# Optimization experiments

Hardware: AMD Instinct MI355X
Metric: run time of the kernel (lower is better)

Reference implementation:

```python
import jax, jax.numpy as jnp
from jax import lax
import numpy as np

B = 2
N_PER = 12000
TIMES = 16
C_IN = 4
# sparse_shape = grid_size[::-1] + [1,0,0], grid_size=[160,160,40]
S1 = (41, 160, 160)
S2 = (21, 80, 80)   # conv2: k3 s2 p1
S3 = (11, 40, 40)   # conv3: k3 s2 p1
S4 = (5, 20, 20)    # conv4: k3 s2 p(0,1,1)
SOUT = (2, 20, 20)  # conv_out: k(3,1,1) s(2,1,1) p0
# per-BN-layer channel counts, flattened into gamma/beta vectors
CH = [16, 16, 32, 32, 32, 64, 64, 64, 64, 64, 64, 128]
OFF = np.concatenate([[0], np.cumsum(CH)]).tolist()


def _downsample_coords(coords, in_shape, k, s, p):
    # spconv SparseConv3d output index rule: output j active iff some active
    # input x satisfies j*s - p <= x <= j*s - p + k - 1 within bounds.
    out_shape = np.array([(in_shape[i] + 2 * p[i] - k[i]) // s[i] + 1 for i in range(3)])
    b, xs = coords[:, :1], coords[:, 1:]
    s_arr = np.array(s)
    cand = []
    for o0 in range(k[0]):
        for o1 in range(k[1]):
            for o2 in range(k[2]):
                j = xs + np.array([p[0] - o0, p[1] - o1, p[2] - o2])
                ok = np.all(j % s_arr == 0, axis=1)
                jj = j // s_arr
                ok &= np.all((jj >= 0) & (jj < out_shape), axis=1)
                cand.append(np.concatenate([b[ok], jj[ok]], axis=1))
    return np.unique(np.concatenate(cand, axis=0), axis=0).astype(np.int32)


def _make_coords():
    rng = np.random.default_rng(0)
    ncell = S1[0] * S1[1] * S1[2]
    per = []
    for b in range(B):
        flat = rng.choice(ncell, size=N_PER, replace=False)
        z, y, x = np.unravel_index(flat, S1)
        per.append(np.stack([np.full(N_PER, b), z, y, x], axis=1))
    c1 = np.concatenate(per, axis=0).astype(np.int32)
    c2 = _downsample_coords(c1, S1, (3, 3, 3), (2, 2, 2), (1, 1, 1))
    c3 = _downsample_coords(c2, S2, (3, 3, 3), (2, 2, 2), (1, 1, 1))
    c4 = _downsample_coords(c3, S3, (3, 3, 3), (2, 2, 2), (0, 1, 1))
    c5 = _downsample_coords(c4, S4, (3, 1, 1), (2, 1, 1), (0, 0, 0))
    return c1, c2, c3, c4, c5


def _w(key, shape):
    fan_in = shape[0] * shape[1] * shape[2] * shape[3]
    return jax.random.normal(key, shape, jnp.float32) * np.float32(np.sqrt(2.0 / fan_in))


def setup_inputs():
    c1, c2, c3, c4, c5 = _make_coords()
    ks = jax.random.split(jax.random.key(0), 16)
    t = TIMES
    return {
        "voxel_features": jax.random.normal(ks[0], (c1.shape[0], C_IN), jnp.float32),
        "w_in": _w(ks[1], (3, 3, 3, C_IN, t)),
        "w1": _w(ks[2], (3, 3, 3, t, t)),
        "w2_0": _w(ks[3], (3, 3, 3, t, 2 * t)),
        "w2_1": _w(ks[4], (3, 3, 3, 2 * t, 2 * t)),
        "w2_2": _w(ks[5], (3, 3, 3, 2 * t, 2 * t)),
        "w3_0": _w(ks[6], (3, 3, 3, 2 * t, 4 * t)),
        "w3_1": _w(ks[7], (3, 3, 3, 4 * t, 4 * t)),
        "w3_2": _w(ks[8], (3, 3, 3, 4 * t, 4 * t)),
        "w4_0": _w(ks[9], (3, 3, 3, 4 * t, 4 * t)),
        "w4_1": _w(ks[10], (3, 3, 3, 4 * t, 4 * t)),
        "w4_2": _w(ks[11], (3, 3, 3, 4 * t, 4 * t)),
        "w_out": _w(ks[12], (3, 1, 1, 4 * t, 8 * t)),
        "gamma": 1.0 + 0.1 * jax.random.normal(ks[13], (sum(CH),), jnp.float32),
        "beta": 0.1 * jax.random.normal(ks[14], (sum(CH),), jnp.float32),
        "coords1": jnp.asarray(c1), "coords2": jnp.asarray(c2),
        "coords3": jnp.asarray(c3), "coords4": jnp.asarray(c4),
        "coords_out": jnp.asarray(c5),
    }


def _sp_conv(feats, in_coords, w, in_shape, out_coords, stride, padding):
    # spconv's rulebook gather->matmul->scatter over active sites computes the
    # same values as a dense conv on a zero-filled grid, read back only at the
    # active output coordinates (subm: out_coords == in_coords).
    dense = jnp.zeros((B,) + in_shape + (feats.shape[1],), feats.dtype)
    dense = dense.at[in_coords[:, 0], in_coords[:, 1], in_coords[:, 2], in_coords[:, 3]].set(feats)
    out = lax.conv_general_dilated(dense, w, window_strides=stride,
                                   padding=[(p, p) for p in padding],
                                   dimension_numbers=("NDHWC", "DHWIO", "NDHWC"))
    return out[out_coords[:, 0], out_coords[:, 1], out_coords[:, 2], out_coords[:, 3]]


def _bn_relu(x, g, b):
    # nn.BatchNorm1d(eps=1e-3) in training mode over the active voxels, + ReLU
    mu = jnp.mean(x, axis=0)
    var = jnp.mean(jnp.square(x - mu), axis=0)
    return jax.nn.relu((x - mu) * (g * lax.rsqrt(var + 1e-3)) + b)


def _forward(voxel_features, ws, gamma, beta, c1, c2, c3, c4, c5):
    layers = [
        (0, c1, S1, c1, (1, 1, 1), (1, 1, 1)),   # conv_input (subm, 4->16)
        (1, c1, S1, c1, (1, 1, 1), (1, 1, 1)),   # conv1 (subm)
        (2, c1, S1, c2, (2, 2, 2), (1, 1, 1)),   # conv2 spconv s2
        (3, c2, S2, c2, (1, 1, 1), (1, 1, 1)),
        (4, c2, S2, c2, (1, 1, 1), (1, 1, 1)),
        (5, c2, S2, c3, (2, 2, 2), (1, 1, 1)),   # conv3 spconv s2
        (6, c3, S3, c3, (1, 1, 1), (1, 1, 1)),
        (7, c3, S3, c3, (1, 1, 1), (1, 1, 1)),
        (8, c3, S3, c4, (2, 2, 2), (0, 1, 1)),   # conv4 spconv s2, pad (0,1,1)
        (9, c4, S4, c4, (1, 1, 1), (1, 1, 1)),
        (10, c4, S4, c4, (1, 1, 1), (1, 1, 1)),
        (11, c4, S4, c5, (2, 1, 1), (0, 0, 0)),  # conv_out k(3,1,1) s(2,1,1)
    ]
    x = voxel_features
    for i, ci, si, co, st, pd in layers:
        x = _sp_conv(x, ci, ws[i], si, co, st, pd)
        x = _bn_relu(x, gamma[OFF[i]:OFF[i + 1]], beta[OFF[i]:OFF[i + 1]])
    return x  # encoded_spconv_tensor features, [N_out, 8*times]


def reference(voxel_features, w_in, w1, w2_0, w2_1, w2_2, w3_0, w3_1, w3_2,
              w4_0, w4_1, w4_2, w_out, gamma, beta,
              coords1, coords2, coords3, coords4, coords_out):
    ws = [w_in, w1, w2_0, w2_1, w2_2, w3_0, w3_1, w3_2, w4_0, w4_1, w4_2, w_out]
    return _forward(voxel_features, ws, gamma, beta,
                    coords1, coords2, coords3, coords4, coords_out)
```

## Files before the change

### kernel.cpp

```cpp
#include <hip/hip_runtime.h>
#include <hip/hip_bf16.h>


typedef __attribute__((ext_vector_type(8))) short bf16x8;
typedef __attribute__((ext_vector_type(4))) short bf16x4s;
typedef __attribute__((ext_vector_type(4))) float f32x4;

typedef const __attribute__((address_space(1))) unsigned int* gas_ptr;
typedef __attribute__((address_space(3))) unsigned int* las_ptr;

__device__ __forceinline__ void dma16(const unsigned short* g, unsigned short* l) {
    __builtin_amdgcn_global_load_lds((gas_ptr)g, (las_ptr)l, 16, 0, 0);
}

__device__ inline unsigned short f2bf(float f) {
    unsigned u = __builtin_bit_cast(unsigned, f);
    u += 0x7FFFu + ((u >> 16) & 1u);
    return (unsigned short)(u >> 16);
}

struct ScatterArgs {
    const int* coords[4];
    int* grid[4];
    int n[4];
    int D[4], H[4], W[4];
};

__global__ __launch_bounds__(256) void scatter_grid_all(ScatterArgs a) {
    const int l = blockIdx.y;
    const int i = blockIdx.x * 256 + threadIdx.x;
    if (i >= a.n[l]) return;
    const int* c = a.coords[l] + 4 * i;
    a.grid[l][((c[0] * a.D[l] + c[1]) * a.H[l] + c[2]) * a.W[l] + c[3]] = i;
}

struct PrepArgs {
    const float* src[11];
    unsigned short* dst[11];
    int T[11], CIN[11], COUT[11], total[11];
};

__global__ __launch_bounds__(256) void prep_w_all(PrepArgs a) {
    const int l = blockIdx.y;
    const int i = blockIdx.x * 256 + threadIdx.x;
    if (i >= a.total[l]) return;
    const int COUT = a.COUT[l], CIN = a.CIN[l], T = a.T[l];
    const int co = i % COUT; const int r = i / COUT; const int ci = r % CIN; const int t = r / CIN;
    unsigned short v = (t < T) ? f2bf(a.src[l][i]) : (unsigned short)0;
    a.dst[l][((size_t)t * COUT + co) * CIN + ci] = v;
}

__global__ __launch_bounds__(256, 4) void sp_conv0(const float* __restrict__ fin,
                                                   const int* __restrict__ grid,
                                                   const int* __restrict__ oc, int n_out,
                                                   const float* __restrict__ w,
                                                   float* __restrict__ out,
                                                   int D, int H, int W) {
    const int c = threadIdx.x & 15;
    const int p = (blockIdx.x * 256 + threadIdx.x) >> 4;
    if (p >= n_out) return;
    const int b   = oc[4*p+0];
    const int iz0 = oc[4*p+1] - 1;
    const int iy0 = oc[4*p+2] - 1;
    const int ix0 = oc[4*p+3] - 1;
    const int* gb = grid + b * (D * H * W);
    float acc = 0.f;
    for (int kd = 0; kd < 3; ++kd) {
        const int iz = iz0 + kd;
        if ((unsigned)iz >= (unsigned)D) continue;
        for (int kh = 0; kh < 3; ++kh) {
            const int iy = iy0 + kh;
            if ((unsigned)iy >= (unsigned)H) continue;
            for (int kw = 0; kw < 3; ++kw) {
                const int ix = ix0 + kw;
                if ((unsigned)ix >= (unsigned)W) continue;
                const int idx = gb[(iz*H + iy)*W + ix];
                if (idx < 0) continue;
                const float4 v = *(const float4*)(fin + (size_t)idx * 4);
                const float* wp = w + (size_t)((kd*3 + kh)*3 + kw) * 64 + c;
                acc = fmaf(v.x, wp[0],  acc);
                acc = fmaf(v.y, wp[16], acc);
                acc = fmaf(v.z, wp[32], acc);
                acc = fmaf(v.w, wp[48], acc);
            }
        }
    }
    out[(size_t)p*16 + c] = acc;
}

template<int COUT>
__global__ __launch_bounds__(256, 4) void sp_conv_lds16(
    const unsigned short* __restrict__ fin, const int* __restrict__ grid,
    const int* __restrict__ oc, int n_out,
    const unsigned short* __restrict__ wt, float* __restrict__ out,
    float* __restrict__ stats,
    int D, int H, int W, int sz, int sy, int sx, int pz, int py, int px)
{
    constexpr int T  = 27;
    constexpr int BT = 4;
    constexpr int TP = 28;
    constexpr int NT = COUT/16;
    constexpr int NB = (COUT == 16) ? BT/2 : BT;

    __shared__ unsigned short Abuf[4*BT*16*16];
    __shared__ unsigned short Bbuf[BT*COUT*16];
    __shared__ float ls[2*COUT];

    const int l     = threadIdx.x & 63;
    const int w     = threadIdx.x >> 6;
    const int n     = l & 15;
    const int quad  = l >> 4;
    const int pbase = blockIdx.x * 64 + w * 16;

    if (threadIdx.x < 2*COUT) ls[threadIdx.x] = 0.f;

    int idx[TP];
    if (quad == 0) {
        int pc = pbase + n;
        if (pc > n_out - 1) pc = n_out - 1;
        const int4 cc = ((const int4*)oc)[pc];
        const int* gb = grid + cc.x * (D * H * W);
        const int iz0 = cc.y * sz - pz;
        const int iy0 = cc.z * sy - py;
        const int ix0 = cc.w * sx - px;
#pragma unroll
        for (int tap = 0; tap < TP; ++tap) {
            const int te = tap < T ? tap : 0;
            const int kd = te/9, kr = te%9, kh = kr/3, kw = kr%3;
            const int iz = iz0 + kd, iy = iy0 + kh, ix = ix0 + kw;
            const bool ok = (tap < T) && (unsigned)iz < (unsigned)D &&
                            (unsigned)iy < (unsigned)H && (unsigned)ix < (unsigned)W;
            const int cz = iz < 0 ? 0 : (iz >= D ? D-1 : iz);
            const int cy = iy < 0 ? 0 : (iy >= H ? H-1 : iy);
            const int cx = ix < 0 ? 0 : (ix >= W ? W-1 : ix);
            const int g = gb[(cz*H + cy)*W + cx];
            idx[tap] = ok ? g : -1;
        }
    }

    f32x4 acc[NT];
#pragma unroll
    for (int t = 0; t < NT; ++t) acc[t] = (f32x4){0.f, 0.f, 0.f, 0.f};

    const int h  = l >> 5;
    const int m  = (l >> 1) & 15;
    const int ch = l & 1;

#pragma unroll
    for (int tb0 = 0; tb0 < TP; tb0 += BT) {
#pragma unroll
        for (int q = 0; q < BT/2; ++q) {
            const int v0 = __shfl(idx[tb0 + 2*q],     m);
            const int v1 = __shfl(idx[tb0 + 2*q + 1], m);
            const int row = h ? v1 : v0;
            const unsigned short* gp = fin + (ptrdiff_t)row*16 + ch*8;
            unsigned short* lp = Abuf + (w*BT + 2*q)*16*16;
            dma16(gp, lp);
        }
        for (int q = w; q < NB; q += 4) {
            if constexpr (COUT == 16) {
                const int tap = tb0 + 2*q + h;
                const int tw = tap < T ? tap : T;
                const unsigned short* gp = wt + ((size_t)tw*COUT + m)*16 + ch*8;
                unsigned short* lp = Bbuf + (2*q)*COUT*16;
                dma16(gp, lp);
            } else {
                const int tap = tb0 + q;
                const int tw = tap < T ? tap : T;
                const int r = l >> 1;
                const unsigned short* gp = wt + ((size_t)tw*COUT + r)*16 + ch*8;
                unsigned short* lp = Bbuf + q*COUT*16;
                dma16(gp, lp);
            }
        }
        __syncthreads();
#pragma unroll
        for (int jp = 0; jp < BT/2; ++jp) {
            const int ts = 2*jp + (quad >> 1);
            bf16x8 a = *(const bf16x8*)(Abuf + ((w*BT + ts)*16 + n)*16 + (quad & 1)*8);
#pragma unroll
            for (int t = 0; t < NT; ++t) {
                bf16x8 b = *(const bf16x8*)(Bbuf + (ts*COUT + t*16 + n)*16 + (quad & 1)*8);
                acc[t] = __builtin_amdgcn_mfma_f32_16x16x32_bf16(a, b, acc[t], 0, 0, 0);
            }
        }
        __syncthreads();
    }

#pragma unroll
    for (int t = 0; t < NT; ++t)
#pragma unroll
        for (int r = 0; r < 4; ++r) {
            const int p = pbase + quad*4 + r;
            if (p < n_out) out[(size_t)p * COUT + t*16 + n] = acc[t][r];
        }

#pragma unroll
    for (int t = 0; t < NT; ++t) {
        float s1 = 0.f, s2 = 0.f;
#pragma unroll
        for (int r = 0; r < 4; ++r) {
            const int p = pbase + quad*4 + r;
            if (p < n_out) { const float v = acc[t][r]; s1 += v; s2 += v*v; }
        }
        s1 += __shfl_xor(s1, 16); s2 += __shfl_xor(s2, 16);
        s1 += __shfl_xor(s1, 32); s2 += __shfl_xor(s2, 32);
        if (quad == 0) {
            atomicAdd(&ls[t*16 + n], s1);
            atomicAdd(&ls[COUT + t*16 + n], s2);
        }
    }
    __syncthreads();
    if (threadIdx.x < 2*COUT) atomicAdd(&stats[threadIdx.x], ls[threadIdx.x]);
}

template<int CIN, int COUT, int BT, int KD, int KH, int KW>
__global__ __launch_bounds__(256, 2) void sp_conv_lds(
    const unsigned short* __restrict__ fin, const int* __restrict__ grid,
    const int* __restrict__ oc, int n_out,
    const unsigned short* __restrict__ wt, float* __restrict__ out,
    float* __restrict__ stats,
    int D, int H, int W, int sz, int sy, int sx, int pz, int py, int px)
{
    constexpr int T    = KD*KH*KW;
    constexpr int TP   = ((T + BT - 1)/BT)*BT;
    constexpr int NT   = COUT/16;
    constexpr int S    = CIN/32;
    constexpr int LPR  = CIN/8;
    constexpr int RPD  = 64/LPR;
    constexpr int ADMA = 16/RPD;
    constexpr int BDMA = COUT/RPD;

    __shared__ unsigned short Abuf[4*BT*16*CIN];
    __shared__ unsigned short Bbuf[BT*COUT*CIN];
    __shared__ float ls[2*COUT];

    const int l     = threadIdx.x & 63;
    const int w     = threadIdx.x >> 6;
    const int n     = l & 15;
    const int quad  = l >> 4;
    const int pbase = blockIdx.x * 64 + w * 16;

    if (threadIdx.x < 2*COUT) ls[threadIdx.x] = 0.f;

    int idx[TP];
    if (quad == 0) {
        int pc = pbase + n;
        if (pc > n_out - 1) pc = n_out - 1;
        const int4 cc = ((const int4*)oc)[pc];
        const int* gb = grid + cc.x * (D * H * W);
        const int iz0 = cc.y * sz - pz;
        const int iy0 = cc.z * sy - py;
        const int ix0 = cc.w * sx - px;
#pragma unroll
        for (int tap = 0; tap < TP; ++tap) {
            const int te = tap < T ? tap : 0;
            const int kd = te/(KH*KW), kr = te%(KH*KW), kh = kr/KW, kw = kr%KW;
            const int iz = iz0 + kd, iy = iy0 + kh, ix = ix0 + kw;
            const bool ok = (tap < T) && (unsigned)iz < (unsigned)D &&
                            (unsigned)iy < (unsigned)H && (unsigned)ix < (unsigned)W;
            const int cz = iz < 0 ? 0 : (iz >= D ? D-1 : iz);
            const int cy = iy < 0 ? 0 : (iy >= H ? H-1 : iy);
            const int cx = ix < 0 ? 0 : (ix >= W ? W-1 : ix);
            const int g = gb[(cz*H + cy)*W + cx];
            idx[tap] = ok ? g : -1;
        }
    }

    f32x4 acc[NT];
#pragma unroll
    for (int t = 0; t < NT; ++t) acc[t] = (f32x4){0.f, 0.f, 0.f, 0.f};

#pragma unroll
    for (int tb0 = 0; tb0 < TP; tb0 += BT) {
#pragma unroll
        for (int j = 0; j < BT; ++j) {
#pragma unroll
            for (int d = 0; d < ADMA; ++d) {
                const int m  = d*RPD + l/LPR;
                const int i0 = __shfl(idx[tb0+j], m);
                const int slot = (l % LPR) ^ (m % LPR);
                const unsigned short* gp = fin + (ptrdiff_t)i0*CIN + slot*8;
                unsigned short* lp = Abuf + ((w*BT + j)*16 + d*RPD)*CIN;
                dma16(gp, lp);
            }
        }
        for (int q = w; q < BT*BDMA; q += 4) {
            const int j = q / BDMA, d = q % BDMA;
            const int t = tb0 + j;
            const int tw = t < T ? t : T;
            const int r  = d*RPD + l/LPR;
            const int slot = (l % LPR) ^ (r % LPR);
            const unsigned short* gp = wt + ((size_t)tw*COUT + r)*CIN + slot*8;
            unsigned short* lp = Bbuf + (j*COUT + d*RPD)*CIN;
            dma16(gp, lp);
        }
        __syncthreads();
#pragma unroll
        for (int j = 0; j < BT; ++j) {
            const unsigned short* Aw = Abuf + (w*BT + j)*16*CIN;
            const unsigned short* Bw = Bbuf + j*COUT*CIN;
#pragma unroll
            for (int s = 0; s < S; ++s) {
                const int c = s*4 + quad;
                bf16x8 a = *(const bf16x8*)(Aw + n*CIN + ((c ^ (n % LPR)) * 8));
#pragma unroll
                for (int t = 0; t < NT; ++t) {
                    const int r = t*16 + n;
                    bf16x8 b = *(const bf16x8*)(Bw + r*CIN + ((c ^ (r % LPR)) * 8));
                    acc[t] = __builtin_amdgcn_mfma_f32_16x16x32_bf16(a, b, acc[t], 0, 0, 0);
                }
            }
        }
        __syncthreads();
    }

#pragma unroll
    for (int t = 0; t < NT; ++t)
#pragma unroll
        for (int r = 0; r < 4; ++r) {
            const int p = pbase + quad*4 + r;
            if (p < n_out) out[(size_t)p * COUT + t*16 + n] = acc[t][r];
        }

#pragma unroll
    for (int t = 0; t < NT; ++t) {
        float s1 = 0.f, s2 = 0.f;
#pragma unroll
        for (int r = 0; r < 4; ++r) {
            const int p = pbase + quad*4 + r;
            if (p < n_out) { const float v = acc[t][r]; s1 += v; s2 += v*v; }
        }
        s1 += __shfl_xor(s1, 16); s2 += __shfl_xor(s2, 16);
        s1 += __shfl_xor(s1, 32); s2 += __shfl_xor(s2, 32);
        if (quad == 0) {
            atomicAdd(&ls[t*16 + n], s1);
            atomicAdd(&ls[COUT + t*16 + n], s2);
        }
    }
    __syncthreads();
    if (threadIdx.x < 2*COUT) atomicAdd(&stats[threadIdx.x], ls[threadIdx.x]);
}

template<int C>
__global__ __launch_bounds__(256) void reduce_stats(const float* __restrict__ x, int nn,
                                                    float* __restrict__ stats)
{
    constexpr int R = 256 / C;
    __shared__ float s1[256];
    __shared__ float s2[256];
    const int c = threadIdx.x % C;
    const int r = threadIdx.x / C;
    float a1 = 0.f, a2 = 0.f;
    for (int i = blockIdx.x * R + r; i < nn; i += R * gridDim.x) {
        float v = x[(size_t)i*C + c];
        a1 += v;
        a2 += v * v;
    }
    s1[threadIdx.x] = a1;
    s2[threadIdx.x] = a2;
    __syncthreads();
    for (int off = 128; off >= C; off >>= 1) {
        if (threadIdx.x < off) {
            s1[threadIdx.x] += s1[threadIdx.x + off];
            s2[threadIdx.x] += s2[threadIdx.x + off];
        }
        __syncthreads();
    }
    if (threadIdx.x < C) {
        atomicAdd(&stats[c],     s1[threadIdx.x]);
        atomicAdd(&stats[C + c], s2[threadIdx.x]);
    }
}

__device__ inline void stv4(float* p, float4 v) { *(float4*)p = v; }
__device__ inline void stv4(unsigned short* p, float4 v) {
    bf16x4s o;
    o.x = (short)f2bf(v.x); o.y = (short)f2bf(v.y);
    o.z = (short)f2bf(v.z); o.w = (short)f2bf(v.w);
    *(bf16x4s*)p = o;
}

template<int C, typename OUT>
__global__ __launch_bounds__(256) void bn_relu_apply(const float* __restrict__ x,
                                                     OUT* __restrict__ y, int nn,
                                                     const float* __restrict__ stats,
                                                     const float* __restrict__ gamma,
                                                     const float* __restrict__ beta)
{
    const size_t q = (size_t)blockIdx.x * blockDim.x + threadIdx.x;
    if (q >= (size_t)nn * (C/4)) return;
    const int c = (int)(q % (size_t)(C/4)) * 4;
    const float inv_n = 1.f / (float)nn;
    const float4 xv = *(const float4*)(x + q*4);
    const float4 s1 = *(const float4*)(stats + c);
    const float4 s2 = *(const float4*)(stats + C + c);
    const float4 gm = *(const float4*)(gamma + c);
    const float4 bt = *(const float4*)(beta + c);
    float4 o;
    { float mu=s1.x*inv_n, var=s2.x*inv_n-mu*mu, g=gm.x*rsqrtf(var+1e-3f);
      float v=(xv.x-mu)*g+bt.x; o.x = v>0.f? v:0.f; }
    { float mu=s1.y*inv_n, var=s2.y*inv_n-mu*mu, g=gm.y*rsqrtf(var+1e-3f);
      float v=(xv.y-mu)*g+bt.y; o.y = v>0.f? v:0.f; }
    { float mu=s1.z*inv_n, var=s2.z*inv_n-mu*mu, g=gm.z*rsqrtf(var+1e-3f);
      float v=(xv.z-mu)*g+bt.z; o.z = v>0.f? v:0.f; }
    { float mu=s1.w*inv_n, var=s2.w*inv_n-mu*mu, g=gm.w*rsqrtf(var+1e-3f);
      float v=(xv.w-mu)*g+bt.w; o.w = v>0.f? v:0.f; }
    stv4(y + q*4, o);
}

extern "C" void kernel_launch(void* const* d_in, const int* in_sizes, int n_in,
                              void* d_out, int out_size, void* d_ws, size_t ws_size,
                              hipStream_t stream) {
    const float* WPTR[12] = {
        (const float*)d_in[1], (const float*)d_in[2], (const float*)d_in[3],
        (const float*)d_in[4], (const float*)d_in[5], (const float*)d_in[6],
        (const float*)d_in[7], (const float*)d_in[8], (const float*)d_in[9],
        (const float*)d_in[10], (const float*)d_in[11], (const float*)d_in[12] };
    const float* vf    = (const float*)d_in[0];
    const float* gamma = (const float*)d_in[13];
    const float* beta  = (const float*)d_in[14];
    const int* c1 = (const int*)d_in[15];
    const int* c2 = (const int*)d_in[16];
    const int* c3 = (const int*)d_in[17];
    const int* c4 = (const int*)d_in[18];
    const int* c5 = (const int*)d_in[19];
    const int N1 = in_sizes[15] / 4;
    const int N2 = in_sizes[16] / 4;
    const int N3 = in_sizes[17] / 4;
    const int N4 = in_sizes[18] / 4;
    const int N5 = in_sizes[19] / 4;

    static const int LT[12]  = {27,27,27,27,27,27,27,27,27,27,27,3};
    static const int LCI[12] = {4,16,16,32,32,32,64,64,64,64,64,64};
    static const int LCO[12] = {16,16,32,32,32,64,64,64,64,64,64,128};

    const size_t G1 = (size_t)2*41*160*160;
    const size_t G2 = (size_t)2*21*80*80;
    const size_t G3 = (size_t)2*11*40*40;
    const size_t G4 = (size_t)2*5*20*20;
    int* grid1 = (int*)d_ws;
    int* grid2 = grid1 + G1;
    int* grid3 = grid2 + G2;
    int* grid4 = grid3 + G3;
    float* stats = (float*)(grid4 + G4);

    size_t maxE = (size_t)N1*16;
    if ((size_t)N2*32  > maxE) maxE = (size_t)N2*32;
    if ((size_t)N3*64  > maxE) maxE = (size_t)N3*64;
    if ((size_t)N4*64  > maxE) maxE = (size_t)N4*64;
    if ((size_t)N5*128 > maxE) maxE = (size_t)N5*128;
    maxE = (maxE + 7) & ~(size_t)7;

    float* raw = stats + 12*256;
    unsigned short* padA = (unsigned short*)(raw + maxE);
    unsigned short* fA   = padA + 128;
    unsigned short* padB = fA + maxE;
    unsigned short* fB   = padB + 128;
    unsigned short* wtb  = fB + maxE;
    size_t wtoff[12];
    {
        size_t o = 0;
        for (int i = 1; i < 12; ++i) {
            wtoff[i] = o;
            o += (size_t)(LT[i] + 1) * LCI[i] * LCO[i];
        }
    }

    hipMemsetAsync(grid1, 0xFF, (G1+G2+G3+G4)*sizeof(int), stream);
    hipMemsetAsync(stats, 0, 12*256*sizeof(float), stream);
    hipMemsetAsync(padA, 0, 128*sizeof(unsigned short), stream);
    hipMemsetAsync(padB, 0, 128*sizeof(unsigned short), stream);

    {
        ScatterArgs sa;
        sa.coords[0]=c1; sa.coords[1]=c2; sa.coords[2]=c3; sa.coords[3]=c4;
        sa.grid[0]=grid1; sa.grid[1]=grid2; sa.grid[2]=grid3; sa.grid[3]=grid4;
        sa.n[0]=N1; sa.n[1]=N2; sa.n[2]=N3; sa.n[3]=N4;
        sa.D[0]=41; sa.H[0]=160; sa.W[0]=160;
        sa.D[1]=21; sa.H[1]= 80; sa.W[1]= 80;
        sa.D[2]=11; sa.H[2]= 40; sa.W[2]= 40;
        sa.D[3]= 5; sa.H[3]= 20; sa.W[3]= 20;
        int mx = N1; if (N2>mx) mx=N2; if (N3>mx) mx=N3; if (N4>mx) mx=N4;
        dim3 g((mx + 255)/256, 4);
        scatter_grid_all<<<g, 256, 0, stream>>>(sa);
    }
    {
        PrepArgs pa;
        int mx = 0;
        for (int i = 1; i < 12; ++i) {
            pa.src[i-1] = WPTR[i];
            pa.dst[i-1] = wtb + wtoff[i];
            pa.T[i-1] = LT[i]; pa.CIN[i-1] = LCI[i]; pa.COUT[i-1] = LCO[i];
            pa.total[i-1] = (LT[i]+1)*LCI[i]*LCO[i];
            if (pa.total[i-1] > mx) mx = pa.total[i-1];
        }
        dim3 g((mx + 255)/256, 11);
        prep_w_all<<<g, 256, 0, stream>>>(pa);
    }

    enum { GOFF_0 = 0, GOFF_1 = 16, GOFF_2 = 32, GOFF_3 = 64, GOFF_4 = 96, GOFF_5 = 128,
           GOFF_6 = 192, GOFF_7 = 256, GOFF_8 = 320, GOFF_9 = 384, GOFF_10 = 448, GOFF_11 = 512 };

#define APPLY(i, COUT, NP, FOUT_T, FOUT) \
    bn_relu_apply<COUT, FOUT_T><<<(((size_t)(NP)*(COUT)/4) + 255)/256, 256, 0, stream>>>( \
        raw, FOUT, NP, stats + (i)*256, gamma + GOFF_##i, beta + GOFF_##i);

    sp_conv0<<<((size_t)N1*16 + 255)/256, 256, 0, stream>>>(vf, grid1, c1, N1, WPTR[0], raw, 41,160,160);
    { int rb = (N1 + 15)/16; if (rb > 240) rb = 240;
      reduce_stats<16><<<rb, 256, 0, stream>>>(raw, N1, stats + 0*256); }
    APPLY(0, 16, N1, unsigned short, fA);

#define CONVS(i, COUT, FIN, GRD, OC, NP, D,H,W, SZ,SY,SX, PZ,PY,PX) \
    sp_conv_lds16<COUT><<<((NP)+63)/64, 256, 0, stream>>>( \
        FIN, GRD, OC, NP, wtb + wtoff[i], raw, stats + (i)*256, D,H,W, SZ,SY,SX, PZ,PY,PX);

#define CONVL(i, CIN, COUT, BT, KD,KH,KW, FIN, GRD, OC, NP, D,H,W, SZ,SY,SX, PZ,PY,PX) \
    sp_conv_lds<CIN,COUT,BT,KD,KH,KW><<<((NP)+63)/64, 256, 0, stream>>>( \
        FIN, GRD, OC, NP, wtb + wtoff[i], raw, stats + (i)*256, D,H,W, SZ,SY,SX, PZ,PY,PX);

    CONVS( 1, 16,       fA, grid1, c1, N1, 41,160,160, 1,1,1, 1,1,1); APPLY( 1, 16, N1, unsigned short, fB);
    CONVS( 2, 32,       fB, grid1, c2, N2, 41,160,160, 2,2,2, 1,1,1); APPLY( 2, 32, N2, unsigned short, fA);
    CONVL ( 3, 32, 32, 7, 3,3,3, fA, grid2, c2, N2, 21, 80, 80, 1,1,1, 1,1,1); APPLY( 3, 32, N2, unsigned short, fB);
    CONVL ( 4, 32, 32, 7, 3,3,3, fB, grid2, c2, N2, 21, 80, 80, 1,1,1, 1,1,1); APPLY( 4, 32, N2, unsigned short, fA);
    CONVL ( 5, 32, 64, 7, 3,3,3, fA, grid2, c3, N3, 21, 80, 80, 2,2,2, 1,1,1); APPLY( 5, 64, N3, unsigned short, fB);
    CONVL ( 6, 64, 64, 3, 3,3,3, fB, grid3, c3, N3, 11, 40, 40, 1,1,1, 1,1,1); APPLY( 6, 64, N3, unsigned short, fA);
    CONVL ( 7, 64, 64, 3, 3,3,3, fA, grid3, c3, N3, 11, 40, 40, 1,1,1, 1,1,1); APPLY( 7, 64, N3, unsigned short, fB);
    CONVL ( 8, 64, 64, 3, 3,3,3, fB, grid3, c4, N4, 11, 40, 40, 2,2,2, 0,1,1); APPLY( 8, 64, N4, unsigned short, fA);
    CONVL ( 9, 64, 64, 3, 3,3,3, fA, grid4, c4, N4,  5, 20, 20, 1,1,1, 1,1,1); APPLY( 9, 64, N4, unsigned short, fB);
    CONVL (10, 64, 64, 3, 3,3,3, fB, grid4, c4, N4,  5, 20, 20, 1,1,1, 1,1,1); APPLY(10, 64, N4, unsigned short, fA);
    CONVL (11, 64,128, 1, 3,1,1, fA, grid4, c5, N5,  5, 20, 20, 2,1,1, 0,0,0); APPLY(11, 128, N5, float, (float*)d_out);
#undef CONVS
#undef CONVL
#undef APPLY
}
```

Baseline: 409.1 us.

## Double-buffer LDS tap batches in sparse conv kernels to overlap DMA with MFMA

Both gathered sparse-conv kernels now hold two LDS buffers for A and B. The next tap batch is issued via global_load_lds DMA while the current batch is consumed by MFMAs, which removes the trailing barrier per batch. To fit the doubled LDS, tap batch sizes are reduced (7→4, 3→2) and launch-bound occupancy hints are made per-layer. The added cost is more loop iterations, and possibly lower occupancy for the larger layers.

```diff
diff --git a/kernel.cpp b/kernel.cpp
--- a/kernel.cpp
+++ b/kernel.cpp
@@ -101,9 +101,12 @@
     constexpr int TP = 28;
     constexpr int NT = COUT/16;
     constexpr int NB = (COUT == 16) ? BT/2 : BT;
-
-    __shared__ unsigned short Abuf[4*BT*16*16];
-    __shared__ unsigned short Bbuf[BT*COUT*16];
+    constexpr int NBATCH = TP/BT;
+    constexpr int ASZ = 4*BT*16*16;
+    constexpr int BSZ = BT*COUT*16;
+
+    __shared__ unsigned short Abuf[2*ASZ];
+    __shared__ unsigned short Bbuf[2*BSZ];
     __shared__ float ls[2*COUT];
 
     const int l     = threadIdx.x & 63;
@@ -146,15 +149,14 @@
     const int m  = (l >> 1) & 15;
     const int ch = l & 1;
 
-#pragma unroll
-    for (int tb0 = 0; tb0 < TP; tb0 += BT) {
+    auto stage = [&](int buf, int tb0) {
 #pragma unroll
         for (int q = 0; q < BT/2; ++q) {
             const int v0 = __shfl(idx[tb0 + 2*q],     m);
             const int v1 = __shfl(idx[tb0 + 2*q + 1], m);
             const int row = h ? v1 : v0;
             const unsigned short* gp = fin + (ptrdiff_t)row*16 + ch*8;
-            unsigned short* lp = Abuf + (w*BT + 2*q)*16*16;
+            unsigned short* lp = Abuf + buf*ASZ + (w*BT + 2*q)*16*16;
             dma16(gp, lp);
         }
         for (int q = w; q < NB; q += 4) {
@@ -162,29 +164,35 @@
                 const int tap = tb0 + 2*q + h;
                 const int tw = tap < T ? tap : T;
                 const unsigned short* gp = wt + ((size_t)tw*COUT + m)*16 + ch*8;
-                unsigned short* lp = Bbuf + (2*q)*COUT*16;
+                unsigned short* lp = Bbuf + buf*BSZ + (2*q)*COUT*16;
                 dma16(gp, lp);
             } else {
                 const int tap = tb0 + q;
                 const int tw = tap < T ? tap : T;
                 const int r = l >> 1;
                 const unsigned short* gp = wt + ((size_t)tw*COUT + r)*16 + ch*8;
-                unsigned short* lp = Bbuf + q*COUT*16;
+                unsigned short* lp = Bbuf + buf*BSZ + q*COUT*16;
                 dma16(gp, lp);
             }
         }
+    };
+
+    stage(0, 0);
+#pragma unroll
+    for (int bt = 0; bt < NBATCH; ++bt) {
+        const int cur = bt & 1;
         __syncthreads();
+        if (bt + 1 < NBATCH) stage(cur ^ 1, (bt + 1)*BT);
 #pragma unroll
         for (int jp = 0; jp < BT/2; ++jp) {
             const int ts = 2*jp + (quad >> 1);
-            bf16x8 a = *(const bf16x8*)(Abuf + ((w*BT + ts)*16 + n)*16 + (quad & 1)*8);
+            bf16x8 a = *(const bf16x8*)(Abuf + cur*ASZ + ((w*BT + ts)*16 + n)*16 + (quad & 1)*8);
 #pragma unroll
             for (int t = 0; t < NT; ++t) {
-                bf16x8 b = *(const bf16x8*)(Bbuf + (ts*COUT + t*16 + n)*16 + (quad & 1)*8);
+                bf16x8 b = *(const bf16x8*)(Bbuf + cur*BSZ + (ts*COUT + t*16 + n)*16 + (quad & 1)*8);
                 acc[t] = __builtin_amdgcn_mfma_f32_16x16x32_bf16(a, b, acc[t], 0, 0, 0);
             }
         }
-        __syncthreads();
     }
 
 #pragma unroll
@@ -214,8 +222,8 @@
     if (threadIdx.x < 2*COUT) atomicAdd(&stats[threadIdx.x], ls[threadIdx.x]);
 }
 
-template<int CIN, int COUT, int BT, int KD, int KH, int KW>
-__global__ __launch_bounds__(256, 2) void sp_conv_lds(
+template<int CIN, int COUT, int BT, int KD, int KH, int KW, int MB>
+__global__ __launch_bounds__(256, MB) void sp_conv_lds(
     const unsigned short* __restrict__ fin, const int* __restrict__ grid,
     const int* __restrict__ oc, int n_out,
     const unsigned short* __restrict__ wt, float* __restrict__ out,
@@ -223,16 +231,19 @@
     int D, int H, int W, int sz, int sy, int sx, int pz, int py, int px)
 {
     constexpr int T    = KD*KH*KW;
-    constexpr int TP   = ((T + BT - 1)/BT)*BT;
+    constexpr int NBATCH = (T + BT - 1)/BT;
+    constexpr int TP   = NBATCH*BT;
     constexpr int NT   = COUT/16;
     constexpr int S    = CIN/32;
     constexpr int LPR  = CIN/8;
     constexpr int RPD  = 64/LPR;
     constexpr int ADMA = 16/RPD;
     constexpr int BDMA = COUT/RPD;
-
-    __shared__ unsigned short Abuf[4*BT*16*CIN];
-    __shared__ unsigned short Bbuf[BT*COUT*CIN];
+    constexpr int ASZ  = 4*BT*16*CIN;
+    constexpr int BSZ  = BT*COUT*CIN;
+
+    __shared__ unsigned short Abuf[2*ASZ];
+    __shared__ unsigned short Bbuf[2*BSZ];
     __shared__ float ls[2*COUT];
 
     const int l     = threadIdx.x & 63;
@@ -271,8 +282,9 @@
 #pragma unroll
     for (int t = 0; t < NT; ++t) acc[t] = (f32x4){0.f, 0.f, 0.f, 0.f};
 
-#pragma unroll
-    for (int tb0 = 0; tb0 < TP; tb0 += BT) {
+    auto stage = [&](int buf, int tb0) {
+        unsigned short* Ab = Abuf + buf*ASZ;
+        unsigned short* Bb = Bbuf + buf*BSZ;
 #pragma unroll
         for (int j = 0; j < BT; ++j) {
 #pragma unroll
@@ -281,7 +293,7 @@
                 const int i0 = __shfl(idx[tb0+j], m);
                 const int slot = (l % LPR) ^ (m % LPR);
                 const unsigned short* gp = fin + (ptrdiff_t)i0*CIN + slot*8;
-                unsigned short* lp = Abuf + ((w*BT + j)*16 + d*RPD)*CIN;
+                unsigned short* lp = Ab + ((w*BT + j)*16 + d*RPD)*CIN;
                 dma16(gp, lp);
             }
         }
@@ -292,14 +304,21 @@
             const int r  = d*RPD + l/LPR;
             const int slot = (l % LPR) ^ (r % LPR);
             const unsigned short* gp = wt + ((size_t)tw*COUT + r)*CIN + slot*8;
-            unsigned short* lp = Bbuf + (j*COUT + d*RPD)*CIN;
+            unsigned short* lp = Bb + (j*COUT + d*RPD)*CIN;
             dma16(gp, lp);
         }
+    };
+
+    stage(0, 0);
+#pragma unroll
+    for (int bt = 0; bt < NBATCH; ++bt) {
+        const int cur = bt & 1;
         __syncthreads();
+        if (bt + 1 < NBATCH) stage(cur ^ 1, (bt + 1)*BT);
 #pragma unroll
         for (int j = 0; j < BT; ++j) {
-            const unsigned short* Aw = Abuf + (w*BT + j)*16*CIN;
-            const unsigned short* Bw = Bbuf + j*COUT*CIN;
+            const unsigned short* Aw = Abuf + cur*ASZ + (w*BT + j)*16*CIN;
+            const unsigned short* Bw = Bbuf + cur*BSZ + j*COUT*CIN;
 #pragma unroll
             for (int s = 0; s < S; ++s) {
                 const int c = s*4 + quad;
@@ -312,7 +331,6 @@
                 }
             }
         }
-        __syncthreads();
     }
 
 #pragma unroll
@@ -515,21 +533,21 @@
     sp_conv_lds16<COUT><<<((NP)+63)/64, 256, 0, stream>>>( \
         FIN, GRD, OC, NP, wtb + wtoff[i], raw, stats + (i)*256, D,H,W, SZ,SY,SX, PZ,PY,PX);
 
-#define CONVL(i, CIN, COUT, BT, KD,KH,KW, FIN, GRD, OC, NP, D,H,W, SZ,SY,SX, PZ,PY,PX) \
-    sp_conv_lds<CIN,COUT,BT,KD,KH,KW><<<((NP)+63)/64, 256, 0, stream>>>( \
+#define CONVL(i, CIN, COUT, BT, MB, KD,KH,KW, FIN, GRD, OC, NP, D,H,W, SZ,SY,SX, PZ,PY,PX) \
+    sp_conv_lds<CIN,COUT,BT,KD,KH,KW,MB><<<((NP)+63)/64, 256, 0, stream>>>( \
         FIN, GRD, OC, NP, wtb + wtoff[i], raw, stats + (i)*256, D,H,W, SZ,SY,SX, PZ,PY,PX);
 
     CONVS( 1, 16,       fA, grid1, c1, N1, 41,160,160, 1,1,1, 1,1,1); APPLY( 1, 16, N1, unsigned short, fB);
     CONVS( 2, 32,       fB, grid1, c2, N2, 41,160,160, 2,2,2, 1,1,1); APPLY( 2, 32, N2, unsigned short, fA);
-    CONVL ( 3, 32, 32, 7, 3,3,3, fA, grid2, c2, N2, 21, 80, 80, 1,1,1, 1,1,1); APPLY( 3, 32, N2, unsigned short, fB);
-    CONVL ( 4, 32, 32, 7, 3,3,3, fB, grid2, c2, N2, 21, 80, 80, 1,1,1, 1,1,1); APPLY( 4, 32, N2, unsigned short, fA);
-    CONVL ( 5, 32, 64, 7, 3,3,3, fA, grid2, c3, N3, 21, 80, 80, 2,2,2, 1,1,1); APPLY( 5, 64, N3, unsigned short, fB);
-    CONVL ( 6, 64, 64, 3, 3,3,3, fB, grid3, c3, N3, 11, 40, 40, 1,1,1, 1,1,1); APPLY( 6, 64, N3, unsigned short, fA);
-    CONVL ( 7, 64, 64, 3, 3,3,3, fA, grid3, c3, N3, 11, 40, 40, 1,1,1, 1,1,1); APPLY( 7, 64, N3, unsigned short, fB);
-    CONVL ( 8, 64, 64, 3, 3,3,3, fB, grid3, c4, N4, 11, 40, 40, 2,2,2, 0,1,1); APPLY( 8, 64, N4, unsigned short, fA);
-    CONVL ( 9, 64, 64, 3, 3,3,3, fA, grid4, c4, N4,  5, 20, 20, 1,1,1, 1,1,1); APPLY( 9, 64, N4, unsigned short, fB);
-    CONVL (10, 64, 64, 3, 3,3,3, fB, grid4, c4, N4,  5, 20, 20, 1,1,1, 1,1,1); APPLY(10, 64, N4, unsigned short, fA);
-    CONVL (11, 64,128, 1, 3,1,1, fA, grid4, c5, N5,  5, 20, 20, 2,1,1, 0,0,0); APPLY(11, 128, N5, float, (float*)d_out);
+    CONVL ( 3, 32, 32, 4, 3, 3,3,3, fA, grid2, c2, N2, 21, 80, 80, 1,1,1, 1,1,1); APPLY( 3, 32, N2, unsigned short, fB);
+    CONVL ( 4, 32, 32, 4, 3, 3,3,3, fB, grid2, c2, N2, 21, 80, 80, 1,1,1, 1,1,1); APPLY( 4, 32, N2, unsigned short, fA);
+    CONVL ( 5, 32, 64, 4, 2, 3,3,3, fA, grid2, c3, N3, 21, 80, 80, 2,2,2, 1,1,1); APPLY( 5, 64, N3, unsigned short, fB);
+    CONVL ( 6, 64, 64, 2, 2, 3,3,3, fB, grid3, c3, N3, 11, 40, 40, 1,1,1, 1,1,1); APPLY( 6, 64, N3, unsigned short, fA);
+    CONVL ( 7, 64, 64, 2, 2, 3,3,3, fA, grid3, c3, N3, 11, 40, 40, 1,1,1, 1,1,1); APPLY( 7, 64, N3, unsigned short, fB);
+    CONVL ( 8, 64, 64, 2, 2, 3,3,3, fB, grid3, c4, N4, 11, 40, 40, 2,2,2, 0,1,1); APPLY( 8, 64, N4, unsigned short, fA);
+    CONVL ( 9, 64, 64, 2, 2, 3,3,3, fA, grid4, c4, N4,  5, 20, 20, 1,1,1, 1,1,1); APPLY( 9, 64, N4, unsigned short, fB);
+    CONVL (10, 64, 64, 2, 2, 3,3,3, fB, grid4, c4, N4,  5, 20, 20, 1,1,1, 1,1,1); APPLY(10, 64, N4, unsigned short, fA);
+    CONVL (11, 64,128, 1, 3, 3,1,1, fA, grid4, c5, N5,  5, 20, 20, 2,1,1, 0,0,0); APPLY(11, 128, N5, float, (float*)d_out);
 #undef CONVS
 #undef CONVL
 #undef APPLY
```

New measurement: 440.9 us. +7.8%, slower.

## Replace LDS-staged gather with direct global loads into MFMA operands

Applied to the files above, without the earlier changes.

Both sparse conv kernels drop the shared-memory staging of gathered input rows and weights via global_load_lds and the per-tap-block barriers. Each lane now computes its own rulebook indices and loads its bf16x8 A and B fragments straight from global memory into registers for the MFMA. This removes LDS traffic and __syncthreads stalls and lets occupancy rise (launch bounds raised to 4 waves per SIMD for the larger kernel). The trade-off is that all quads now do the grid lookups redundantly, and weight fragments are re-read from global or cache by every wave instead of being shared through LDS.

```diff
diff --git a/kernel.cpp b/kernel.cpp
--- a/kernel.cpp
+++ b/kernel.cpp
@@ -5,13 +5,6 @@
 typedef __attribute__((ext_vector_type(8))) short bf16x8;
 typedef __attribute__((ext_vector_type(4))) short bf16x4s;
 typedef __attribute__((ext_vector_type(4))) float f32x4;
-
-typedef const __attribute__((address_space(1))) unsigned int* gas_ptr;
-typedef __attribute__((address_space(3))) unsigned int* las_ptr;
-
-__device__ __forceinline__ void dma16(const unsigned short* g, unsigned short* l) {
-    __builtin_amdgcn_global_load_lds((gas_ptr)g, (las_ptr)l, 16, 0, 0);
-}
 
 __device__ inline unsigned short f2bf(float f) {
     unsigned u = __builtin_bit_cast(unsigned, f);
@@ -89,7 +82,7 @@
 }
 
 template<int COUT>
-__global__ __launch_bounds__(256, 4) void sp_conv_lds16(
+__global__ __launch_bounds__(256, 4) void sp_conv_dir16(
     const unsigned short* __restrict__ fin, const int* __restrict__ grid,
     const int* __restrict__ oc, int n_out,
     const unsigned short* __restrict__ wt, float* __restrict__ out,
@@ -97,13 +90,9 @@
     int D, int H, int W, int sz, int sy, int sx, int pz, int py, int px)
 {
     constexpr int T  = 27;
-    constexpr int BT = 4;
     constexpr int TP = 28;
     constexpr int NT = COUT/16;
-    constexpr int NB = (COUT == 16) ? BT/2 : BT;
-
-    __shared__ unsigned short Abuf[4*BT*16*16];
-    __shared__ unsigned short Bbuf[BT*COUT*16];
+
     __shared__ float ls[2*COUT];
 
     const int l     = threadIdx.x & 63;
@@ -114,77 +103,48 @@
 
     if (threadIdx.x < 2*COUT) ls[threadIdx.x] = 0.f;
 
+    int pc = pbase + n;
+    if (pc > n_out - 1) pc = n_out - 1;
+    const int4 cc = ((const int4*)oc)[pc];
+    const int* gb = grid + cc.x * (D * H * W);
+    const int iz0 = cc.y * sz - pz;
+    const int iy0 = cc.z * sy - py;
+    const int ix0 = cc.w * sx - px;
+
     int idx[TP];
-    if (quad == 0) {
-        int pc = pbase + n;
-        if (pc > n_out - 1) pc = n_out - 1;
-        const int4 cc = ((const int4*)oc)[pc];
-        const int* gb = grid + cc.x * (D * H * W);
-        const int iz0 = cc.y * sz - pz;
-        const int iy0 = cc.z * sy - py;
-        const int ix0 = cc.w * sx - px;
-#pragma unroll
-        for (int tap = 0; tap < TP; ++tap) {
-            const int te = tap < T ? tap : 0;
-            const int kd = te/9, kr = te%9, kh = kr/3, kw = kr%3;
-            const int iz = iz0 + kd, iy = iy0 + kh, ix = ix0 + kw;
-            const bool ok = (tap < T) && (unsigned)iz < (unsigned)D &&
-                            (unsigned)iy < (unsigned)H && (unsigned)ix < (unsigned)W;
-            const int cz = iz < 0 ? 0 : (iz >= D ? D-1 : iz);
-            const int cy = iy < 0 ? 0 : (iy >= H ? H-1 : iy);
-            const int cx = ix < 0 ? 0 : (ix >= W ? W-1 : ix);
-            const int g = gb[(cz*H + cy)*W + cx];
-            idx[tap] = ok ? g : -1;
-        }
+#pragma unroll
+    for (int tap = 0; tap < TP; ++tap) {
+        const int te = tap < T ? tap : 0;
+        const int kd = te/9, kr = te%9, kh = kr/3, kw = kr%3;
+        const int iz = iz0 + kd, iy = iy0 + kh, ix = ix0 + kw;
+        const bool ok = (tap < T) && (unsigned)iz < (unsigned)D &&
+                        (unsigned)iy < (unsigned)H && (unsigned)ix < (unsigned)W;
+        const int cz = iz < 0 ? 0 : (iz >= D ? D-1 : iz);
+        const int cy = iy < 0 ? 0 : (iy >= H ? H-1 : iy);
+        const int cx = ix < 0 ? 0 : (ix >= W ? W-1 : ix);
+        const int g = gb[(cz*H + cy)*W + cx];
+        idx[tap] = ok ? g : -1;
     }
 
     f32x4 acc[NT];
 #pragma unroll
     for (int t = 0; t < NT; ++t) acc[t] = (f32x4){0.f, 0.f, 0.f, 0.f};
 
-    const int h  = l >> 5;
-    const int m  = (l >> 1) & 15;
-    const int ch = l & 1;
-
-#pragma unroll
-    for (int tb0 = 0; tb0 < TP; tb0 += BT) {
-#pragma unroll
-        for (int q = 0; q < BT/2; ++q) {
-            const int v0 = __shfl(idx[tb0 + 2*q],     m);
-            const int v1 = __shfl(idx[tb0 + 2*q + 1], m);
-            const int row = h ? v1 : v0;
-            const unsigned short* gp = fin + (ptrdiff_t)row*16 + ch*8;
-            unsigned short* lp = Abuf + (w*BT + 2*q)*16*16;
-            dma16(gp, lp);
-        }
-        for (int q = w; q < NB; q += 4) {
-            if constexpr (COUT == 16) {
-                const int tap = tb0 + 2*q + h;
-                const int tw = tap < T ? tap : T;
-                const unsigned short* gp = wt + ((size_t)tw*COUT + m)*16 + ch*8;
-                unsigned short* lp = Bbuf + (2*q)*COUT*16;
-                dma16(gp, lp);
-            } else {
-                const int tap = tb0 + q;
-                const int tw = tap < T ? tap : T;
-                const int r = l >> 1;
-                const unsigned short* gp = wt + ((size_t)tw*COUT + r)*16 + ch*8;
-                unsigned short* lp = Bbuf + q*COUT*16;
-                dma16(gp, lp);
-            }
-        }
-        __syncthreads();
-#pragma unroll
-        for (int jp = 0; jp < BT/2; ++jp) {
-            const int ts = 2*jp + (quad >> 1);
-            bf16x8 a = *(const bf16x8*)(Abuf + ((w*BT + ts)*16 + n)*16 + (quad & 1)*8);
-#pragma unroll
-            for (int t = 0; t < NT; ++t) {
-                bf16x8 b = *(const bf16x8*)(Bbuf + (ts*COUT + t*16 + n)*16 + (quad & 1)*8);
-                acc[t] = __builtin_amdgcn_mfma_f32_16x16x32_bf16(a, b, acc[t], 0, 0, 0);
-            }
-        }
-        __syncthreads();
+    const int th  = quad >> 1;
+    const int chh = (quad & 1) * 8;
+
+#pragma unroll
+    for (int p = 0; p < TP/2; ++p) {
+        const int i0 = idx[2*p];
+        const int i1 = idx[2*p + 1];
+        const int row = th ? i1 : i0;
+        const int tw  = 2*p + th;
+        bf16x8 a = *(const bf16x8*)(fin + (ptrdiff_t)row*16 + chh);
+#pragma unroll
+        for (int t = 0; t < NT; ++t) {
+            bf16x8 b = *(const bf16x8*)(wt + ((size_t)tw*COUT + t*16 + n)*16 + chh);
+            acc[t] = __builtin_amdgcn_mfma_f32_16x16x32_bf16(a, b, acc[t], 0, 0, 0);
+        }
     }
 
 #pragma unroll
@@ -195,6 +155,7 @@
             if (p < n_out) out[(size_t)p * COUT + t*16 + n] = acc[t][r];
         }
 
+    __syncthreads();
 #pragma unroll
     for (int t = 0; t < NT; ++t) {
         float s1 = 0.f, s2 = 0.f;
@@ -214,25 +175,18 @@
     if (threadIdx.x < 2*COUT) atomicAdd(&stats[threadIdx.x], ls[threadIdx.x]);
 }
 
-template<int CIN, int COUT, int BT, int KD, int KH, int KW>
-__global__ __launch_bounds__(256, 2) void sp_conv_lds(
+template<int CIN, int COUT, int KD, int KH, int KW>
+__global__ __launch_bounds__(256, 4) void sp_conv_dir(
     const unsigned short* __restrict__ fin, const int* __restrict__ grid,
     const int* __restrict__ oc, int n_out,
     const unsigned short* __restrict__ wt, float* __restrict__ out,
     float* __restrict__ stats,
     int D, int H, int W, int sz, int sy, int sx, int pz, int py, int px)
 {
-    constexpr int T    = KD*KH*KW;
-    constexpr int TP   = ((T + BT - 1)/BT)*BT;
-    constexpr int NT   = COUT/16;
-    constexpr int S    = CIN/32;
-    constexpr int LPR  = CIN/8;
-    constexpr int RPD  = 64/LPR;
-    constexpr int ADMA = 16/RPD;
-    constexpr int BDMA = COUT/RPD;
-
-    __shared__ unsigned short Abuf[4*BT*16*CIN];
-    __shared__ unsigned short Bbuf[BT*COUT*CIN];
+    constexpr int T  = KD*KH*KW;
+    constexpr int NT = COUT/16;
+    constexpr int S  = CIN/32;
+
     __shared__ float ls[2*COUT];
 
     const int l     = threadIdx.x & 63;
@@ -243,28 +197,26 @@
 
     if (threadIdx.x < 2*COUT) ls[threadIdx.x] = 0.f;
 
-    int idx[TP];
-    if (quad == 0) {
-        int pc = pbase + n;
-        if (pc > n_out - 1) pc = n_out - 1;
-        const int4 cc = ((const int4*)oc)[pc];
-        const int* gb = grid + cc.x * (D * H * W);
-        const int iz0 = cc.y * sz - pz;
-        const int iy0 = cc.z * sy - py;
-        const int ix0 = cc.w * sx - px;
-#pragma unroll
-        for (int tap = 0; tap < TP; ++tap) {
-            const int te = tap < T ? tap : 0;
-            const int kd = te/(KH*KW), kr = te%(KH*KW), kh = kr/KW, kw = kr%KW;
-            const int iz = iz0 + kd, iy = iy0 + kh, ix = ix0 + kw;
-            const bool ok = (tap < T) && (unsigned)iz < (unsigned)D &&
-                            (unsigned)iy < (unsigned)H && (unsigned)ix < (unsigned)W;
-            const int cz = iz < 0 ? 0 : (iz >= D ? D-1 : iz);
-            const int cy = iy < 0 ? 0 : (iy >= H ? H-1 : iy);
-            const int cx = ix < 0 ? 0 : (ix >= W ? W-1 : ix);
-            const int g = gb[(cz*H + cy)*W + cx];
-            idx[tap] = ok ? g : -1;
-        }
+    int pc = pbase + n;
+    if (pc > n_out - 1) pc = n_out - 1;
+    const int4 cc = ((const int4*)oc)[pc];
+    const int* gb = grid + cc.x * (D * H * W);
+    const int iz0 = cc.y * sz - pz;
+    const int iy0 = cc.z * sy - py;
+    const int ix0 = cc.w * sx - px;
+
+    int idx[T];
+#pragma unroll
+    for (int tap = 0; tap < T; ++tap) {
+        const int kd = tap/(KH*KW), kr = tap%(KH*KW), kh = kr/KW, kw = kr%KW;
+        const int iz = iz0 + kd, iy = iy0 + kh, ix = ix0 + kw;
+        const bool ok = (unsigned)iz < (unsigned)D &&
+                        (unsigned)iy < (unsigned)H && (unsigned)ix < (unsigned)W;
+        const int cz = iz < 0 ? 0 : (iz >= D ? D-1 : iz);
+        const int cy = iy < 0 ? 0 : (iy >= H ? H-1 : iy);
+        const int cx = ix < 0 ? 0 : (ix >= W ? W-1 : ix);
+        const int g = gb[(cz*H + cy)*W + cx];
+        idx[tap] = ok ? g : -1;
     }
 
     f32x4 acc[NT];
@@ -272,47 +224,18 @@
     for (int t = 0; t < NT; ++t) acc[t] = (f32x4){0.f, 0.f, 0.f, 0.f};
 
 #pragma unroll
-    for (int tb0 = 0; tb0 < TP; tb0 += BT) {
-#pragma unroll
-        for (int j = 0; j < BT; ++j) {
-#pragma unroll
-            for (int d = 0; d < ADMA; ++d) {
-                const int m  = d*RPD + l/LPR;
-                const int i0 = __shfl(idx[tb0+j], m);
-                const int slot = (l % LPR) ^ (m % LPR);
-                const unsigned short* gp = fin + (ptrdiff_t)i0*CIN + slot*8;
-                unsigned short* lp = Abuf + ((w*BT + j)*16 + d*RPD)*CIN;
-                dma16(gp, lp);
+    for (int tap = 0; tap < T; ++tap) {
+        const unsigned short* ap = fin + (ptrdiff_t)idx[tap] * CIN;
+        const unsigned short* bp = wt + ((size_t)tap * COUT + n) * CIN;
+#pragma unroll
+        for (int s = 0; s < S; ++s) {
+            bf16x8 a = *(const bf16x8*)(ap + s*32 + quad*8);
+#pragma unroll
+            for (int t = 0; t < NT; ++t) {
+                bf16x8 b = *(const bf16x8*)(bp + (size_t)t*16*CIN + s*32 + quad*8);
+                acc[t] = __builtin_amdgcn_mfma_f32_16x16x32_bf16(a, b, acc[t], 0, 0, 0);
             }
         }
-        for (int q = w; q < BT*BDMA; q += 4) {
-            const int j = q / BDMA, d = q % BDMA;
-            const int t = tb0 + j;
-            const int tw = t < T ? t : T;
-            const int r  = d*RPD + l/LPR;
-            const int slot = (l % LPR) ^ (r % LPR);
-            const unsigned short* gp = wt + ((size_t)tw*COUT + r)*CIN + slot*8;
-            unsigned short* lp = Bbuf + (j*COUT + d*RPD)*CIN;
-            dma16(gp, lp);
-        }
-        __syncthreads();
-#pragma unroll
-        for (int j = 0; j < BT; ++j) {
-            const unsigned short* Aw = Abuf + (w*BT + j)*16*CIN;
-            const unsigned short* Bw = Bbuf + j*COUT*CIN;
-#pragma unroll
-            for (int s = 0; s < S; ++s) {
-                const int c = s*4 + quad;
-                bf16x8 a = *(const bf16x8*)(Aw + n*CIN + ((c ^ (n % LPR)) * 8));
-#pragma unroll
-                for (int t = 0; t < NT; ++t) {
-                    const int r = t*16 + n;
-                    bf16x8 b = *(const bf16x8*)(Bw + r*CIN + ((c ^ (r % LPR)) * 8));
-                    acc[t] = __builtin_amdgcn_mfma_f32_16x16x32_bf16(a, b, acc[t], 0, 0, 0);
-                }
-            }
-        }
-        __syncthreads();
     }
 
 #pragma unroll
@@ -323,6 +246,7 @@
             if (p < n_out) out[(size_t)p * COUT + t*16 + n] = acc[t][r];
         }
 
+    __syncthreads();
 #pragma unroll
     for (int t = 0; t < NT; ++t) {
         float s1 = 0.f, s2 = 0.f;
@@ -512,24 +436,24 @@
     APPLY(0, 16, N1, unsigned short, fA);
 
 #define CONVS(i, COUT, FIN, GRD, OC, NP, D,H,W, SZ,SY,SX, PZ,PY,PX) \
-    sp_conv_lds16<COUT><<<((NP)+63)/64, 256, 0, stream>>>( \
+    sp_conv_dir16<COUT><<<((NP)+63)/64, 256, 0, stream>>>( \
         FIN, GRD, OC, NP, wtb + wtoff[i], raw, stats + (i)*256, D,H,W, SZ,SY,SX, PZ,PY,PX);
 
-#define CONVL(i, CIN, COUT, BT, KD,KH,KW, FIN, GRD, OC, NP, D,H,W, SZ,SY,SX, PZ,PY,PX) \
-    sp_conv_lds<CIN,COUT,BT,KD,KH,KW><<<((NP)+63)/64, 256, 0, stream>>>( \
+#define CONVL(i, CIN, COUT, KD,KH,KW, FIN, GRD, OC, NP, D,H,W, SZ,SY,SX, PZ,PY,PX) \
+    sp_conv_dir<CIN,COUT,KD,KH,KW><<<((NP)+63)/64, 256, 0, stream>>>( \
         FIN, GRD, OC, NP, wtb + wtoff[i], raw, stats + (i)*256, D,H,W, SZ,SY,SX, PZ,PY,PX);
 
     CONVS( 1, 16,       fA, grid1, c1, N1, 41,160,160, 1,1,1, 1,1,1); APPLY( 1, 16, N1, unsigned short, fB);
     CONVS( 2, 32,       fB, grid1, c2, N2, 41,160,160, 2,2,2, 1,1,1); APPLY( 2, 32, N2, unsigned short, fA);
-    CONVL ( 3, 32, 32, 7, 3,3,3, fA, grid2, c2, N2, 21, 80, 80, 1,1,1, 1,1,1); APPLY( 3, 32, N2, unsigned short, fB);
-    CONVL ( 4, 32, 32, 7, 3,3,3, fB, grid2, c2, N2, 21, 80, 80, 1,1,1, 1,1,1); APPLY( 4, 32, N2, unsigned short, fA);
-    CONVL ( 5, 32, 64, 7, 3,3,3, fA, grid2, c3, N3, 21, 80, 80, 2,2,2, 1,1,1); APPLY( 5, 64, N3, unsigned short, fB);
-    CONVL ( 6, 64, 64, 3, 3,3,3, fB, grid3, c3, N3, 11, 40, 40, 1,1,1, 1,1,1); APPLY( 6, 64, N3, unsigned short, fA);
-    CONVL ( 7, 64, 64, 3, 3,3,3, fA, grid3, c3, N3, 11, 40, 40, 1,1,1, 1,1,1); APPLY( 7, 64, N3, unsigned short, fB);
-    CONVL ( 8, 64, 64, 3, 3,3,3, fB, grid3, c4, N4, 11, 40, 40, 2,2,2, 0,1,1); APPLY( 8, 64, N4, unsigned short, fA);
-    CONVL ( 9, 64, 64, 3, 3,3,3, fA, grid4, c4, N4,  5, 20, 20, 1,1,1, 1,1,1); APPLY( 9, 64, N4, unsigned short, fB);
-    CONVL (10, 64, 64, 3, 3,3,3, fB, grid4, c4, N4,  5, 20, 20, 1,1,1, 1,1,1); APPLY(10, 64, N4, unsigned short, fA);
-    CONVL (11, 64,128, 1, 3,1,1, fA, grid4, c5, N5,  5, 20, 20, 2,1,1, 0,0,0); APPLY(11, 128, N5, float, (float*)d_out);
+    CONVL ( 3, 32, 32, 3,3,3, fA, grid2, c2, N2, 21, 80, 80, 1,1,1, 1,1,1); APPLY( 3, 32, N2, unsigned short, fB);
+    CONVL ( 4, 32, 32, 3,3,3, fB, grid2, c2, N2, 21, 80, 80, 1,1,1, 1,1,1); APPLY( 4, 32, N2, unsigned short, fA);
+    CONVL ( 5, 32, 64, 3,3,3, fA, grid2, c3, N3, 21, 80, 80, 2,2,2, 1,1,1); APPLY( 5, 64, N3, unsigned short, fB);
+    CONVL ( 6, 64, 64, 3,3,3, fB, grid3, c3, N3, 11, 40, 40, 1,1,1, 1,1,1); APPLY( 6, 64, N3, unsigned short, fA);
+    CONVL ( 7, 64, 64, 3,3,3, fA, grid3, c3, N3, 11, 40, 40, 1,1,1, 1,1,1); APPLY( 7, 64, N3, unsigned short, fB);
+    CONVL ( 8, 64, 64, 3,3,3, fB, grid3, c4, N4, 11, 40, 40, 2,2,2, 0,1,1); APPLY( 8, 64, N4, unsigned short, fA);
+    CONVL ( 9, 64, 64, 3,3,3, fA, grid4, c4, N4,  5, 20, 20, 1,1,1, 1,1,1); APPLY( 9, 64, N4, unsigned short, fB);
+    CONVL (10, 64, 64, 3,3,3, fB, grid4, c4, N4,  5, 20, 20, 1,1,1, 1,1,1); APPLY(10, 64, N4, unsigned short, fA);
+    CONVL (11, 64,128, 3,1,1, fA, grid4, c5, N5,  5, 20, 20, 2,1,1, 0,0,0); APPLY(11, 128, N5, float, (float*)d_out);
 #undef CONVS
 #undef CONVL
 #undef APPLY
```

Result: slower. 617.9 us (+51.0%).
